# Optimization experiments

Hardware: AMD Instinct MI355X
Metric: run time of the kernel (lower is better)

## Reference

```python
import jax, jax.numpy as jnp
import numpy as np

N = 200_000      # active voxels
INC = 64
OUTC = 96
GRID = 128
EPS = 1e-5


def _build_neighbor_maps():
    """Precompute gather/scatter index maps for the 26 off-center hypercube
    offsets (the 4th kernel dim has size 1, so offsets live in 3D)."""
    rng = np.random.default_rng(0)
    G = GRID ** 3
    lin = rng.choice(G, size=N, replace=False).astype(np.int64)
    z = lin % GRID
    y = (lin // GRID) % GRID
    x = lin // (GRID * GRID)
    lookup = np.full(G, -1, np.int64)
    lookup[lin] = np.arange(N)
    offsets = [(dx, dy, dz) for dx in (-1, 0, 1) for dy in (-1, 0, 1)
               for dz in (-1, 0, 1) if (dx, dy, dz) != (0, 0, 0)]
    pin, pout = [], []
    for dx, dy, dz in offsets:
        nx, ny, nz = x + dx, y + dy, z + dz
        valid = (nx >= 0) & (nx < GRID) & (ny >= 0) & (ny < GRID) & (nz >= 0) & (nz < GRID)
        nlin = (nx * GRID + ny) * GRID + nz
        nb = np.where(valid, lookup[np.clip(nlin, 0, G - 1)], -1)
        m = nb >= 0
        pin.append(np.arange(N)[m])
        pout.append(nb[m])
    pmax = max(len(p) for p in pin)
    in_idx = np.zeros((26, pmax), np.int64)          # pad gathers row 0 (harmless)
    out_idx = np.full((26, pmax), N, np.int64)       # pad scatters to sink row N
    for k, (pi, po) in enumerate(zip(pin, pout)):
        in_idx[k, : len(pi)] = pi
        out_idx[k, : len(po)] = po
    return in_idx, out_idx


def setup_inputs() -> dict:
    in_idx, out_idx = _build_neighbor_maps()
    key = jax.random.key(0)
    k1, k2, k3 = jax.random.split(key, 3)
    std = 1.0 / np.sqrt(INC * 27)
    feats = jax.random.normal(k1, (N, INC), jnp.float32)
    W_center = jax.random.normal(k2, (INC, OUTC), jnp.float32) * std
    W_off = jax.random.normal(k3, (26, INC, OUTC), jnp.float32) * std
    gamma = jnp.ones((OUTC,), jnp.float32)   # bn.weight init to 1.0
    beta = jnp.zeros((OUTC,), jnp.float32)   # bn.bias init to 0.0
    return {"feats": feats, "W_center": W_center, "W_off": W_off,
            "gamma": gamma, "beta": beta,
            "in_idx": jnp.asarray(in_idx), "out_idx": jnp.asarray(out_idx)}


def reference(feats, W_center, W_off, gamma, beta, in_idx, out_idx):
    # --- sparse conv-transpose: gather -> GEMM -> scatter-add ---
    out = feats @ W_center                                   # center offset: identity map, [N, outc]
    gathered = feats[in_idx]                                 # [26, P, inc]
    contrib = jnp.einsum('kpc,kcd->kpd', gathered, W_off)    # [26, P, outc]
    out = jnp.concatenate([out, jnp.zeros((1, OUTC), out.dtype)], axis=0)  # sink row
    out = out.at[out_idx.reshape(-1)].add(contrib.reshape(-1, OUTC))[:N]
    # --- BatchNorm (training-mode batch stats) + ReLU ---
    mean = out.mean(axis=0)
    var = out.var(axis=0)
    y = (out - mean) * jax.lax.rsqrt(var + EPS) * gamma + beta
    return jax.nn.relu(y)
```

## Files before the change

### kernel.cpp

```cpp
#include <hip/hip_runtime.h>


#define N_VOX   200000
#define INC     64
#define OUTC    96
#define NOFF    26
#define NBLK    782
#define NPAD    200192
#define EPSV    1e-5f

using bf16x8 = __attribute__((ext_vector_type(8))) short;
using f32x4  = __attribute__((ext_vector_type(4))) float;

__device__ inline unsigned short f2bf(float x) {
    union { float f; unsigned u; } v; v.f = x;
    unsigned r = (v.u + 0x7FFFu + ((v.u >> 16) & 1u)) >> 16;
    return (unsigned short)r;
}

__global__ void fill_src_kernel(const int* __restrict__ in_idx,
                                const int* __restrict__ out_idx,
                                int P, int* __restrict__ srcmap) {
    int idx = blockIdx.x * blockDim.x + threadIdx.x;
    if (idx >= NOFF * P) return;
    int dst = out_idx[idx];
    if (dst >= N_VOX) return;
    int k = idx / P;
    srcmap[(size_t)k * NPAD + dst] = in_idx[idx];
}

__global__ void wprep_kernel(const float* __restrict__ Wc,
                             const float* __restrict__ Woff,
                             unsigned short* __restrict__ Wb) {
    int t = blockIdx.x * blockDim.x + threadIdx.x;
    if (t >= 27 * 2 * 6 * 64) return;
    int lane = t & 63;
    int g    = t >> 6;
    int ct   = g % 6;
    int s    = (g / 6) % 2;
    int m    = g / 12;
    const float* W = (m == 26) ? Wc : (Woff + (size_t)m * INC * OUTC);
    int k0 = s * 32 + (lane >> 4) * 8;
    int c  = ct * 16 + (lane & 15);
    bf16x8 v;
    #pragma unroll
    for (int e = 0; e < 8; ++e)
        v[e] = (short)f2bf(W[(size_t)(k0 + e) * OUTC + c]);
    *(bf16x8*)(Wb + (size_t)t * 8) = v;
}

__global__ void fcvt_kernel(const float* __restrict__ feats,
                            unsigned short* __restrict__ featsb) {
    int i = blockIdx.x * blockDim.x + threadIdx.x;
    if (i >= N_VOX * INC / 8) return;
    const float4* src = (const float4*)feats + (size_t)i * 2;
    float4 f0 = src[0], f1 = src[1];
    bf16x8 v;
    v[0] = (short)f2bf(f0.x); v[1] = (short)f2bf(f0.y);
    v[2] = (short)f2bf(f0.z); v[3] = (short)f2bf(f0.w);
    v[4] = (short)f2bf(f1.x); v[5] = (short)f2bf(f1.y);
    v[6] = (short)f2bf(f1.z); v[7] = (short)f2bf(f1.w);
    *(bf16x8*)(featsb + (size_t)i * 8) = v;
}

template<int STAGE_BF16>
__global__ __launch_bounds__(256, 2)
void conv_mfma_kernel(const unsigned short* __restrict__ featsb,
                      const unsigned short* __restrict__ Wb,
                      const int* __restrict__ srcmap,
                      float* __restrict__ outf,
                      unsigned short* __restrict__ stg,
                      float* __restrict__ pstats) {
    __shared__ float sred[768];

    const int t     = threadIdx.x;
    const int wid   = t >> 6;
    const int lane  = t & 63;
    const int blk   = blockIdx.x;
    const int rbase = blk * 256 + wid * 64;
    const int row16 = lane & 15;
    const int kgrp  = lane >> 4;

    f32x4  acc[4][6] = {};
    bf16x8 aC[4][2], aN[4][2];
    int smC[4], smN[4];
    int hasC, hasN;

    #pragma unroll
    for (int rt = 0; rt < 4; ++rt)
        smC[rt] = srcmap[rbase + rt * 16 + row16];
    #pragma unroll
    for (int rt = 0; rt < 4; ++rt) {
        int row = rbase + rt * 16 + row16;
        int src = row < N_VOX ? row : N_VOX;
        const unsigned short* fr = featsb + (size_t)src * INC + kgrp * 8;
        aC[rt][0] = *(const bf16x8*)fr;
        aC[rt][1] = *(const bf16x8*)(fr + 32);
    }
    hasC = 0xF;

    #pragma unroll 1
    for (int idx = 0; idx < 27; ++idx) {
        if (idx < 25) {
            #pragma unroll
            for (int rt = 0; rt < 4; ++rt)
                smN[rt] = srcmap[(size_t)(idx + 1) * NPAD + rbase + rt * 16 + row16];
        }

        if (idx < 26) {
            int h = 0;
            #pragma unroll
            for (int rt = 0; rt < 4; ++rt) {
                int s = smC[rt];
                if (__ballot(s >= 0)) h |= (1 << rt);
                bf16x8 g0 = {}, g1 = {};
                if (s >= 0) {
                    const unsigned short* fr = featsb + (size_t)s * INC + kgrp * 8;
                    g0 = *(const bf16x8*)fr;
                    g1 = *(const bf16x8*)(fr + 32);
                }
                aN[rt][0] = g0; aN[rt][1] = g1;
            }
            hasN = __builtin_amdgcn_readfirstlane(h);
        } else {
            hasN = 0;
        }

        const unsigned short* wb = Wb + (size_t)(idx == 0 ? 26 : idx - 1) * 6144;
        bf16x8 B0[6], B1[6];
        #pragma unroll
        for (int ct = 0; ct < 6; ++ct) {
            B0[ct] = *(const bf16x8*)(wb + (size_t)ct * 512 + lane * 8);
            B1[ct] = *(const bf16x8*)(wb + (size_t)(6 + ct) * 512 + lane * 8);
        }

        #pragma unroll
        for (int rt = 0; rt < 4; ++rt) {
            if (hasC & (1 << rt)) {
                #pragma unroll
                for (int ct = 0; ct < 6; ++ct) {
                    acc[rt][ct] = __builtin_amdgcn_mfma_f32_16x16x32_bf16(aC[rt][0], B0[ct], acc[rt][ct], 0, 0, 0);
                    acc[rt][ct] = __builtin_amdgcn_mfma_f32_16x16x32_bf16(aC[rt][1], B1[ct], acc[rt][ct], 0, 0, 0);
                }
            }
        }

        #pragma unroll
        for (int rt = 0; rt < 4; ++rt) {
            aC[rt][0] = aN[rt][0]; aC[rt][1] = aN[rt][1];
            smC[rt] = (idx < 25) ? smN[rt] : -1;
        }
        hasC = hasN;
    }

    float s6[6], q6[6];
    #pragma unroll
    for (int ct = 0; ct < 6; ++ct) {
        float s = 0.f, q = 0.f;
        #pragma unroll
        for (int rt = 0; rt < 4; ++rt) {
            f32x4 a = acc[rt][ct];
            s += a[0] + a[1] + a[2] + a[3];
            q += a[0]*a[0] + a[1]*a[1] + a[2]*a[2] + a[3]*a[3];
        }
        s += __shfl_xor(s, 16); q += __shfl_xor(q, 16);
        s += __shfl_xor(s, 32); q += __shfl_xor(q, 32);
        s6[ct] = s; q6[ct] = q;
    }
    if (lane < 16) {
        #pragma unroll
        for (int ct = 0; ct < 6; ++ct) {
            sred[wid * 96 + ct * 16 + lane]       = s6[ct];
            sred[384 + wid * 96 + ct * 16 + lane] = q6[ct];
        }
    }
    __syncthreads();
    if (t < 96) {
        float s = sred[t] + sred[96 + t] + sred[192 + t] + sred[288 + t];
        pstats[(size_t)t * NBLK + blk] = s;
    } else if (t < 192) {
        int c = t - 96;
        float q = sred[384 + c] + sred[480 + c] + sred[576 + c] + sred[672 + c];
        pstats[(size_t)(96 + c) * NBLK + blk] = q;
    }

    #pragma unroll
    for (int rt = 0; rt < 4; ++rt) {
        #pragma unroll
        for (int ct = 0; ct < 6; ++ct) {
            #pragma unroll
            for (int j = 0; j < 4; ++j) {
                int row = rbase + rt * 16 + kgrp * 4 + j;
                if (row < N_VOX) {
                    if (STAGE_BF16)
                        stg[(size_t)row * OUTC + ct * 16 + row16] = f2bf(acc[rt][ct][j]);
                    else
                        outf[(size_t)row * OUTC + ct * 16 + row16] = acc[rt][ct][j];
                }
            }
        }
    }
}

__global__ void stats_reduce_kernel(const float* __restrict__ pstats,
                                    const float* __restrict__ gamma,
                                    const float* __restrict__ beta,
                                    float* __restrict__ scsh) {
    int c = blockIdx.x;
    int t = threadIdx.x;
    float s = 0.f, q = 0.f;
    for (int i = t; i < NBLK; i += 256) {
        s += pstats[(size_t)c * NBLK + i];
        q += pstats[(size_t)(96 + c) * NBLK + i];
    }
    #pragma unroll
    for (int d = 1; d < 64; d <<= 1) {
        s += __shfl_xor(s, d);
        q += __shfl_xor(q, d);
    }
    __shared__ float rs[4], rq[4];
    if ((t & 63) == 0) { rs[t >> 6] = s; rq[t >> 6] = q; }
    __syncthreads();
    if (t == 0) {
        s = rs[0] + rs[1] + rs[2] + rs[3];
        q = rq[0] + rq[1] + rq[2] + rq[3];
        float inv_n = 1.0f / (float)N_VOX;
        float mean = s * inv_n;
        float var  = q * inv_n - mean * mean;
        float sc   = gamma[c] * rsqrtf(var + EPSV);
        scsh[c]      = sc;
        scsh[96 + c] = beta[c] - mean * sc;
    }
}

__global__ void apply_bn_bf16_kernel(const unsigned short* __restrict__ stg,
                                     float* __restrict__ out,
                                     const float* __restrict__ scsh) {
    __shared__ float sc[OUTC], sh[OUTC];
    int t = threadIdx.x;
    if (t < OUTC) { sc[t] = scsh[t]; sh[t] = scsh[96 + t]; }
    __syncthreads();
    const int total8 = N_VOX * OUTC / 8;
    for (int i = blockIdx.x * blockDim.x + t; i < total8; i += gridDim.x * blockDim.x) {
        bf16x8 v = *(const bf16x8*)(stg + (size_t)i * 8);
        int c = (i % 12) * 8;
        float o[8];
        #pragma unroll
        for (int j = 0; j < 8; ++j) {
            union { unsigned u; float f; } w; w.u = (unsigned)(unsigned short)v[j] << 16;
            o[j] = fmaxf(fmaf(w.f, sc[c + j], sh[c + j]), 0.f);
        }
        float4* dst = (float4*)(out + (size_t)i * 8);
        dst[0] = make_float4(o[0], o[1], o[2], o[3]);
        dst[1] = make_float4(o[4], o[5], o[6], o[7]);
    }
}

__global__ void apply_bn_fp32_kernel(float* __restrict__ out,
                                     const float* __restrict__ scsh) {
    __shared__ float sc[OUTC], sh[OUTC];
    int t = threadIdx.x;
    if (t < OUTC) { sc[t] = scsh[t]; sh[t] = scsh[96 + t]; }
    __syncthreads();
    const int total4 = N_VOX * OUTC / 4;
    for (int i = blockIdx.x * blockDim.x + t; i < total4; i += gridDim.x * blockDim.x) {
        float4 v = ((float4*)out)[i];
        int c = (i * 4) % OUTC;
        v.x = fmaxf(fmaf(v.x, sc[c    ], sh[c    ]), 0.f);
        v.y = fmaxf(fmaf(v.y, sc[c + 1], sh[c + 1]), 0.f);
        v.z = fmaxf(fmaf(v.z, sc[c + 2], sh[c + 2]), 0.f);
        v.w = fmaxf(fmaf(v.w, sc[c + 3], sh[c + 3]), 0.f);
        ((float4*)out)[i] = v;
    }
}

extern "C" void kernel_launch(void* const* d_in, const int* in_sizes, int n_in,
                              void* d_out, int out_size, void* d_ws, size_t ws_size,
                              hipStream_t stream) {
    const float* feats   = (const float*)d_in[0];
    const float* Wc      = (const float*)d_in[1];
    const float* Woff    = (const float*)d_in[2];
    const float* gamma   = (const float*)d_in[3];
    const float* beta    = (const float*)d_in[4];
    const int*   in_idx  = (const int*)d_in[5];
    const int*   out_idx = (const int*)d_in[6];
    const int P = in_sizes[5] / NOFF;

    char* w = (char*)d_ws;
    int* srcmap = (int*)w;                   w += (size_t)NOFF * NPAD * 4;
    unsigned short* Wb = (unsigned short*)w; w += (size_t)27 * 6144 * 2;
    float* pstats = (float*)w;               w += (size_t)192 * NBLK * 4;
    float* scsh = (float*)w;                 w += 256 * 4;
    unsigned short* featsb = (unsigned short*)w;
    w += (size_t)(N_VOX + 1) * INC * 2;
    unsigned short* stg = (unsigned short*)w;
    size_t need_stg = (size_t)(w - (char*)d_ws) + (size_t)N_VOX * OUTC * 2;
    bool use_stg = (ws_size >= need_stg);

    hipMemsetAsync(srcmap, 0xFF, (size_t)NOFF * NPAD * 4, stream);
    hipMemsetAsync(featsb + (size_t)N_VOX * INC, 0, INC * 2, stream);
    fill_src_kernel<<<(NOFF * P + 255) / 256, 256, 0, stream>>>(in_idx, out_idx, P, srcmap);
    wprep_kernel<<<(27 * 2 * 6 * 64 + 255) / 256, 256, 0, stream>>>(Wc, Woff, Wb);
    fcvt_kernel<<<(N_VOX * INC / 8 + 255) / 256, 256, 0, stream>>>(feats, featsb);

    float* out = (float*)d_out;
    if (use_stg) {
        conv_mfma_kernel<1><<<NBLK, 256, 0, stream>>>(featsb, Wb, srcmap, out, stg, pstats);
        stats_reduce_kernel<<<96, 256, 0, stream>>>(pstats, gamma, beta, scsh);
        apply_bn_bf16_kernel<<<2048, 256, 0, stream>>>(stg, out, scsh);
    } else {
        conv_mfma_kernel<0><<<NBLK, 256, 0, stream>>>(featsb, Wb, srcmap, out, stg, pstats);
        stats_reduce_kernel<<<96, 256, 0, stream>>>(pstats, gamma, beta, scsh);
        apply_bn_fp32_kernel<<<2048, 256, 0, stream>>>(out, scsh);
    }
}
```

Before: 141.5 us.

## Split output columns across waves to halve accumulators and raise occupancy

Each 256-thread block now covers 128 rows instead of 256. Its four waves form a 2x2 grid: two row groups by two 48-column halves. Each wave holds 12 MFMA accumulators instead of 24 and loads only half the weight fragments, and launch bounds rise from 2 to 3 blocks per CU so more waves can hide gather latency. The cost is that every gathered feature row is loaded by two waves, which doubles gather traffic, and the grid doubles to 1563 blocks. The per-block stats reduction and the tail-row validity mask are adjusted to match.

```diff
diff --git a/kernel.cpp b/kernel.cpp
--- a/kernel.cpp
+++ b/kernel.cpp
@@ -5,7 +5,7 @@
 #define INC     64
 #define OUTC    96
 #define NOFF    26
-#define NBLK    782
+#define NBLK    1563
 #define NPAD    200192
 #define EPSV    1e-5f
 
@@ -64,24 +64,27 @@
 }
 
 template<int STAGE_BF16>
-__global__ __launch_bounds__(256, 2)
+__global__ __launch_bounds__(256, 3)
 void conv_mfma_kernel(const unsigned short* __restrict__ featsb,
                       const unsigned short* __restrict__ Wb,
                       const int* __restrict__ srcmap,
                       float* __restrict__ outf,
                       unsigned short* __restrict__ stg,
                       float* __restrict__ pstats) {
-    __shared__ float sred[768];
-
-    const int t     = threadIdx.x;
-    const int wid   = t >> 6;
-    const int lane  = t & 63;
-    const int blk   = blockIdx.x;
-    const int rbase = blk * 256 + wid * 64;
-    const int row16 = lane & 15;
-    const int kgrp  = lane >> 4;
-
-    f32x4  acc[4][6] = {};
+    __shared__ float sred[384];
+
+    const int t      = threadIdx.x;
+    const int wid    = t >> 6;
+    const int lane   = t & 63;
+    const int rowgrp = wid >> 1;
+    const int colgrp = wid & 1;
+    const int blk    = blockIdx.x;
+    const int rbase  = blk * 128 + rowgrp * 64;
+    const int cbase  = colgrp * 48;
+    const int row16  = lane & 15;
+    const int kgrp   = lane >> 4;
+
+    f32x4  acc[4][3] = {};
     bf16x8 aC[4][2], aN[4][2];
     int smC[4], smN[4];
     int hasC, hasN;
@@ -89,15 +92,19 @@
     #pragma unroll
     for (int rt = 0; rt < 4; ++rt)
         smC[rt] = srcmap[rbase + rt * 16 + row16];
-    #pragma unroll
-    for (int rt = 0; rt < 4; ++rt) {
-        int row = rbase + rt * 16 + row16;
-        int src = row < N_VOX ? row : N_VOX;
-        const unsigned short* fr = featsb + (size_t)src * INC + kgrp * 8;
-        aC[rt][0] = *(const bf16x8*)fr;
-        aC[rt][1] = *(const bf16x8*)(fr + 32);
-    }
-    hasC = 0xF;
+    {
+        int h = 0;
+        #pragma unroll
+        for (int rt = 0; rt < 4; ++rt) {
+            int row = rbase + rt * 16 + row16;
+            if (__ballot(row < N_VOX)) h |= (1 << rt);
+            int src = row < N_VOX ? row : N_VOX;
+            const unsigned short* fr = featsb + (size_t)src * INC + kgrp * 8;
+            aC[rt][0] = *(const bf16x8*)fr;
+            aC[rt][1] = *(const bf16x8*)(fr + 32);
+        }
+        hasC = __builtin_amdgcn_readfirstlane(h);
+    }
 
     #pragma unroll 1
     for (int idx = 0; idx < 27; ++idx) {
@@ -126,19 +133,20 @@
             hasN = 0;
         }
 
-        const unsigned short* wb = Wb + (size_t)(idx == 0 ? 26 : idx - 1) * 6144;
-        bf16x8 B0[6], B1[6];
-        #pragma unroll
-        for (int ct = 0; ct < 6; ++ct) {
-            B0[ct] = *(const bf16x8*)(wb + (size_t)ct * 512 + lane * 8);
-            B1[ct] = *(const bf16x8*)(wb + (size_t)(6 + ct) * 512 + lane * 8);
+        const int m = (idx == 0) ? 26 : idx - 1;
+        const unsigned short* wb = Wb + (size_t)m * 6144;
+        bf16x8 B0[3], B1[3];
+        #pragma unroll
+        for (int ct = 0; ct < 3; ++ct) {
+            B0[ct] = *(const bf16x8*)(wb + (size_t)(colgrp * 3 + ct) * 512 + lane * 8);
+            B1[ct] = *(const bf16x8*)(wb + (size_t)(6 + colgrp * 3 + ct) * 512 + lane * 8);
         }
 
         #pragma unroll
         for (int rt = 0; rt < 4; ++rt) {
             if (hasC & (1 << rt)) {
                 #pragma unroll
-                for (int ct = 0; ct < 6; ++ct) {
+                for (int ct = 0; ct < 3; ++ct) {
                     acc[rt][ct] = __builtin_amdgcn_mfma_f32_16x16x32_bf16(aC[rt][0], B0[ct], acc[rt][ct], 0, 0, 0);
                     acc[rt][ct] = __builtin_amdgcn_mfma_f32_16x16x32_bf16(aC[rt][1], B1[ct], acc[rt][ct], 0, 0, 0);
                 }
@@ -153,9 +161,9 @@
         hasC = hasN;
     }
 
-    float s6[6], q6[6];
-    #pragma unroll
-    for (int ct = 0; ct < 6; ++ct) {
+    float s3[3], q3[3];
+    #pragma unroll
+    for (int ct = 0; ct < 3; ++ct) {
         float s = 0.f, q = 0.f;
         #pragma unroll
         for (int rt = 0; rt < 4; ++rt) {
@@ -165,37 +173,37 @@
         }
         s += __shfl_xor(s, 16); q += __shfl_xor(q, 16);
         s += __shfl_xor(s, 32); q += __shfl_xor(q, 32);
-        s6[ct] = s; q6[ct] = q;
+        s3[ct] = s; q3[ct] = q;
     }
     if (lane < 16) {
         #pragma unroll
-        for (int ct = 0; ct < 6; ++ct) {
-            sred[wid * 96 + ct * 16 + lane]       = s6[ct];
-            sred[384 + wid * 96 + ct * 16 + lane] = q6[ct];
+        for (int ct = 0; ct < 3; ++ct) {
+            sred[wid * 48 + ct * 16 + lane]       = s3[ct];
+            sred[192 + wid * 48 + ct * 16 + lane] = q3[ct];
         }
     }
     __syncthreads();
     if (t < 96) {
-        float s = sred[t] + sred[96 + t] + sred[192 + t] + sred[288 + t];
+        int cg = t / 48, cc = t % 48;
+        float s = sred[cg * 48 + cc] + sred[(2 + cg) * 48 + cc];
+        float q = sred[192 + cg * 48 + cc] + sred[192 + (2 + cg) * 48 + cc];
         pstats[(size_t)t * NBLK + blk] = s;
-    } else if (t < 192) {
-        int c = t - 96;
-        float q = sred[384 + c] + sred[480 + c] + sred[576 + c] + sred[672 + c];
-        pstats[(size_t)(96 + c) * NBLK + blk] = q;
+        pstats[(size_t)(96 + t) * NBLK + blk] = q;
     }
 
     #pragma unroll
     for (int rt = 0; rt < 4; ++rt) {
         #pragma unroll
-        for (int ct = 0; ct < 6; ++ct) {
+        for (int ct = 0; ct < 3; ++ct) {
             #pragma unroll
             for (int j = 0; j < 4; ++j) {
                 int row = rbase + rt * 16 + kgrp * 4 + j;
                 if (row < N_VOX) {
+                    int col = cbase + ct * 16 + row16;
                     if (STAGE_BF16)
-                        stg[(size_t)row * OUTC + ct * 16 + row16] = f2bf(acc[rt][ct][j]);
+                        stg[(size_t)row * OUTC + col] = f2bf(acc[rt][ct][j]);
                     else
-                        outf[(size_t)row * OUTC + ct * 16 + row16] = acc[rt][ct][j];
+                        outf[(size_t)row * OUTC + col] = acc[rt][ct][j];
                 }
             }
         }
```

Result: slower. 160.6 us (+13.5%).
